# Kernel optimization log

Measured on AMD Instinct MI355X. Metric: run time of the kernel, lower is better.

Reference implementation:

```python
import jax, jax.numpy as jnp
import numpy as np

N_NODES = 100000
N_EDGES = 1600000
D_FEAT = 48
N_LAYERS = 3  # GCN(n_layers=3) builds exactly 3 GraphConv layers


def setup_inputs() -> dict:
    key = jax.random.key(0)
    k1, k2, k3 = jax.random.split(key, 3)
    features = jax.random.normal(k1, (N_NODES, D_FEAT), dtype=jnp.float32)
    src = jax.random.randint(k2, (N_EDGES,), 0, N_NODES, dtype=jnp.int32)
    dst = jax.random.randint(k3, (N_EDGES,), 0, N_NODES, dtype=jnp.int32)
    return {"features": features, "src": src, "dst": dst}


def reference(features, src, dst):
    # GraphConv(norm='none', weight=False, bias=False): h_v = sum_{u->v} h_u, then activation.
    # Layers 0..N_LAYERS-2 apply relu; the final layer has no activation.
    h = features
    for i in range(N_LAYERS):
        msgs = h[src]  # gather source features per edge: [E, D]
        h = jax.ops.segment_sum(msgs, dst, num_segments=N_NODES)  # scatter-add to dst
        if i < N_LAYERS - 1:
            h = jax.nn.relu(h)
    return h
```

## Files before the change

### kernel.cpp

```cpp
#include <hip/hip_runtime.h>

#define D 48
#define BSH 8
#define BN 256
#define NBMAX 400
#define CH 256
#define CAPT 5120
#define LOUTSZ 6400
#define PB 6400

typedef float v2f __attribute__((ext_vector_type(2)));

#if defined(__has_builtin)
#if __has_builtin(__builtin_amdgcn_cvt_pk_f32_fp8)
#define HAVE_HW_FP8 1
#endif
#if __has_builtin(__builtin_amdgcn_cvt_pk_fp8_f32)
#define HAVE_HW_FP8ENC 1
#endif
#endif

static __device__ inline unsigned int f2bf_rne(float x) {
    unsigned int u = __float_as_uint(x);
    return (u + 0x7FFFu + ((u >> 16) & 1u)) >> 16;
}
static __device__ inline unsigned int pack2(float lo, float hi) {
    return f2bf_rne(lo) | (f2bf_rne(hi) << 16);
}
static __device__ inline float bf_lo(unsigned int u) { return __uint_as_float(u << 16); }
static __device__ inline float bf_hi(unsigned int u) { return __uint_as_float(u & 0xFFFF0000u); }

static __device__ inline unsigned int f2fp8(float x) {
    unsigned int u = __float_as_uint(x);
    unsigned int s = (u >> 24) & 0x80u;
    unsigned int e = (u >> 23) & 0xFFu;
    unsigned int m = u & 0x7FFFFFu;
    if (e < 121u) return s;
    unsigned int m2 = m + 0x7FFFFu + ((m >> 20) & 1u);
    unsigned int carry = m2 >> 23;
    unsigned int e2 = e - 120u + carry;
    unsigned int b = s | (e2 << 3) | ((m2 >> 20) & 7u);
    if (e2 > 15u || (b & 0x7Fu) == 0x7Fu) b = s | 0x7Eu;
    return b;
}
static __device__ inline float fp8_dec(unsigned int b) {
    unsigned int bits = ((b & 0x80u) << 24) | (((b & 0x7Fu) << 20) + (120u << 23));
    float v = __uint_as_float(bits);
    return ((b & 0x7Fu) != 0u) ? v : 0.0f;
}
static __device__ inline unsigned int packfp8x4(float a, float b, float c, float d) {
#if HAVE_HW_FP8ENC
    int w = __builtin_amdgcn_cvt_pk_fp8_f32(a, b, 0, false);
    w = __builtin_amdgcn_cvt_pk_fp8_f32(c, d, w, true);
    return (unsigned int)w;
#else
    return f2fp8(a) | (f2fp8(b) << 8) | (f2fp8(c) << 16) | (f2fp8(d) << 24);
#endif
}


__global__ void k_front(const int* __restrict__ dst, const float* __restrict__ feat,
                        uint2* __restrict__ featq, uint2* __restrict__ h1q,
                        uint4* __restrict__ featb, int* __restrict__ btot,
                        int* __restrict__ cbase, int E, int NB, int CHE, int N) {
    int t = threadIdx.x;
    if (blockIdx.x < CH) {
        int c = blockIdx.x;
        __shared__ int h[NBMAX];
        for (int b = t; b < NB; b += 1024) h[b] = 0;
        __syncthreads();
        int lo = c * CHE, hi = min(lo + CHE, E);
        for (int i = lo + t; i < hi; i += 1024)
            atomicAdd(&h[dst[i] >> BSH], 1);
        __syncthreads();
        for (int b = t; b < NB; b += 1024)
            cbase[c * NB + b] = atomicAdd(&btot[b], h[b]);
    } else {
        if (blockIdx.x == CH && t < 8) {
            h1q[(size_t)N * 8 + t] = make_uint2(0u, 0u);
            featb[(size_t)N * 8 + t] = make_uint4(0u, 0u, 0u, 0u);
        }
        const float4* f4 = (const float4*)feat;
        int total = (N + 1) * 8;
        int i = (blockIdx.x - CH) * 1024 + t;
        int stride = 256 * 1024;
        for (; i < total; i += stride) {
            int node = i >> 3, c = i & 7;
            uint2 v = make_uint2(0u, 0u);
            if (c < 6 && node < N) {
                float4 a = f4[node * 12 + 2 * c];
                float4 b = f4[node * 12 + 2 * c + 1];
                v.x = f2fp8(a.x) | (f2fp8(a.y) << 8) | (f2fp8(a.z) << 16) | (f2fp8(a.w) << 24);
                v.y = f2fp8(b.x) | (f2fp8(b.y) << 8) | (f2fp8(b.z) << 16) | (f2fp8(b.w) << 24);
            }
            featq[i] = v;
        }
    }
}


__global__ void k_scatter(const int* __restrict__ src, const int* __restrict__ dst,
                          const int* __restrict__ btot, const int* __restrict__ cbase,
                          int* __restrict__ stage, int* __restrict__ bbase,
                          int E, int NB, int CHE) {
    int c = blockIdx.x;
    int t = threadIdx.x;
    __shared__ int wtot[8];
    __shared__ int cur[NBMAX];
    int w = t >> 6, ln = t & 63;
    int x = 0, v = 0;
    if (t < 448) {
        v = (t < NB) ? btot[t] : 0;
        x = v;
#pragma unroll
        for (int off = 1; off < 64; off <<= 1) {
            int u = __shfl_up(x, off);
            if (ln >= off) x += u;
        }
        if (ln == 63) wtot[w] = x;
    }
    __syncthreads();
    if (t == 0) {
        int a = 0;
        for (int k = 0; k < 7; k++) { int tmp = wtot[k]; wtot[k] = a; a += tmp; }
        wtot[7] = a;
    }
    __syncthreads();
    if (t < NB) {
        int excl = x - v + wtot[w];
        cur[t] = excl + cbase[c * NB + t];
        if (c == 0) bbase[t] = excl;
    }
    if (c == 0 && t == 0) bbase[NB] = wtot[7];
    __syncthreads();
    int lo = c * CHE, hi = min(lo + CHE, E);
    for (int i = lo + t; i < hi; i += 1024) {
        int s = src[i], d = dst[i];
        int p = atomicAdd(&cur[d >> BSH], 1);
        stage[p] = ((d & (BN - 1)) << 17) | s;
    }
}


__global__ void k_build(const int* __restrict__ stage, const int* __restrict__ bbase,
                        int* __restrict__ row_ptr, int* __restrict__ trips,
                        int* __restrict__ esrc, int N, int NB) {
    int b = blockIdx.x;
    int t = threadIdx.x;
    __shared__ int lbuf[CAPT];
    __shared__ int lout[LOUTSZ];
    __shared__ int hist[BN];
    __shared__ int cur[BN];
    __shared__ int wt[4];
    __shared__ int stot;
    int base = bbase[b];
    int cnt = min(bbase[b + 1] - base, CAPT);
    hist[t] = 0;
    __syncthreads();
    for (int i = t; i < cnt; i += 256) {
        int v = stage[base + i];
        lbuf[i] = v;
        atomicAdd(&hist[v >> 17], 1);
    }
    __syncthreads();
    int orig = hist[t];
    int pc = (orig + 7) & ~7;
    int w = t >> 6, ln = t & 63;
    int x = pc;
#pragma unroll
    for (int off = 1; off < 64; off <<= 1) {
        int u = __shfl_up(x, off);
        if (ln >= off) x += u;
    }
    if (ln == 63) wt[w] = x;
    __syncthreads();
    if (t == 0) {
        int a = 0;
        for (int k = 0; k < 4; k++) { int tmp = wt[k]; wt[k] = a; a += tmp; }
    }
    __syncthreads();
    int ppre = x - pc + wt[w];
    cur[t] = ppre;
    int node = (b << BSH) + t;
    if (node < N) { row_ptr[node] = b * PB + ppre; trips[node] = pc >> 3; }
    for (int k = orig; k < pc; k++) lout[ppre + k] = N;
    if (t == 255) stot = ppre + pc;
    __syncthreads();
    for (int i = t; i < cnt; i += 256) {
        int v = lbuf[i];
        int p = atomicAdd(&cur[v >> 17], 1);
        lout[p] = v & 0x1FFFF;
    }
    __syncthreads();
    int ptot = stot;
    for (int i = t; i < ptot; i += 256) esrc[b * PB + i] = lout[i];
}


#if HAVE_HW_FP8
#define DEC8(q) do { \
        v2f p0 = __builtin_amdgcn_cvt_pk_f32_fp8((int)(q).x, false); \
        v2f p1 = __builtin_amdgcn_cvt_pk_f32_fp8((int)(q).x, true); \
        v2f p2 = __builtin_amdgcn_cvt_pk_f32_fp8((int)(q).y, false); \
        v2f p3 = __builtin_amdgcn_cvt_pk_f32_fp8((int)(q).y, true); \
        a0 += p0.x; a1 += p0.y; a2 += p1.x; a3 += p1.y; \
        a4 += p2.x; a5 += p2.y; a6 += p3.x; a7 += p3.y; } while (0)
#else
#define DEC8(q) do { \
        a0 += fp8_dec((q).x & 0xFFu); a1 += fp8_dec(((q).x >> 8) & 0xFFu); \
        a2 += fp8_dec(((q).x >> 16) & 0xFFu); a3 += fp8_dec((q).x >> 24); \
        a4 += fp8_dec((q).y & 0xFFu); a5 += fp8_dec(((q).y >> 8) & 0xFFu); \
        a6 += fp8_dec(((q).y >> 16) & 0xFFu); a7 += fp8_dec((q).y >> 24); } while (0)
#endif

template <int OUTBF16>
__global__ void k_pullq(const uint2* __restrict__ hin, void* __restrict__ hout,
                        const int* __restrict__ row_ptr, const int* __restrict__ trips,
                        const int* __restrict__ esrc, int n) {
    int grp = threadIdx.x >> 4;
    int lane = threadIdx.x & 15;
    int side = lane >> 3;
    int sub = lane & 7;
    int node = blockIdx.x * 16 + grp;
    if (node >= n) return;
    int j = row_ptr[node];
    int nt = trips[node];
    float a0 = 0.f, a1 = 0.f, a2 = 0.f, a3 = 0.f, a4 = 0.f, a5 = 0.f, a6 = 0.f, a7 = 0.f;
    if (nt > 0) {
        int s0 = esrc[j + 0 + side], s1 = esrc[j + 2 + side];
        int s2 = esrc[j + 4 + side], s3 = esrc[j + 6 + side];
        for (; nt > 0; --nt) {
            uint2 q0 = hin[(size_t)s0 * 8 + sub];
            uint2 q1 = hin[(size_t)s1 * 8 + sub];
            uint2 q2 = hin[(size_t)s2 * 8 + sub];
            uint2 q3 = hin[(size_t)s3 * 8 + sub];
            j += 8;
            int n0 = esrc[j + 0 + side], n1 = esrc[j + 2 + side];
            int n2 = esrc[j + 4 + side], n3 = esrc[j + 6 + side];
            DEC8(q0); DEC8(q1); DEC8(q2); DEC8(q3);
            s0 = n0; s1 = n1; s2 = n2; s3 = n3;
        }
    }
    a0 += __shfl_xor(a0, 8); a1 += __shfl_xor(a1, 8);
    a2 += __shfl_xor(a2, 8); a3 += __shfl_xor(a3, 8);
    a4 += __shfl_xor(a4, 8); a5 += __shfl_xor(a5, 8);
    a6 += __shfl_xor(a6, 8); a7 += __shfl_xor(a7, 8);
    a0 = fmaxf(a0, 0.f); a1 = fmaxf(a1, 0.f); a2 = fmaxf(a2, 0.f); a3 = fmaxf(a3, 0.f);
    a4 = fmaxf(a4, 0.f); a5 = fmaxf(a5, 0.f); a6 = fmaxf(a6, 0.f); a7 = fmaxf(a7, 0.f);
    if (side != 0) return;
    if (OUTBF16) {
        uint4* o = (uint4*)hout + (size_t)node * 8 + sub;
        *o = make_uint4(pack2(a0, a1), pack2(a2, a3), pack2(a4, a5), pack2(a6, a7));
    } else {
        uint2* o = (uint2*)hout + (size_t)node * 8 + sub;
        *o = make_uint2(packfp8x4(a0, a1, a2, a3), packfp8x4(a4, a5, a6, a7));
    }
}
#undef DEC8


__global__ void k_pull(const uint4* __restrict__ hin, float* __restrict__ hout,
                       const int* __restrict__ row_ptr, const int* __restrict__ trips,
                       const int* __restrict__ esrc, int n) {
    int grp = threadIdx.x >> 4;
    int lane = threadIdx.x & 15;
    int side = lane >> 3;
    int sub = lane & 7;
    int node = blockIdx.x * 16 + grp;
    if (node >= n) return;
    int j = row_ptr[node];
    int nt = trips[node];
    float a0 = 0.f, a1 = 0.f, a2 = 0.f, a3 = 0.f, a4 = 0.f, a5 = 0.f, a6 = 0.f, a7 = 0.f;
    if (nt > 0) {
        int s0 = esrc[j + 0 + side], s1 = esrc[j + 2 + side];
        int s2 = esrc[j + 4 + side], s3 = esrc[j + 6 + side];
        for (; nt > 0; --nt) {
            uint4 q0 = hin[(size_t)s0 * 8 + sub];
            uint4 q1 = hin[(size_t)s1 * 8 + sub];
            uint4 q2 = hin[(size_t)s2 * 8 + sub];
            uint4 q3 = hin[(size_t)s3 * 8 + sub];
            j += 8;
            int n0 = esrc[j + 0 + side], n1 = esrc[j + 2 + side];
            int n2 = esrc[j + 4 + side], n3 = esrc[j + 6 + side];
            a0 += bf_lo(q0.x); a1 += bf_hi(q0.x); a2 += bf_lo(q0.y); a3 += bf_hi(q0.y);
            a4 += bf_lo(q0.z); a5 += bf_hi(q0.z); a6 += bf_lo(q0.w); a7 += bf_hi(q0.w);
            a0 += bf_lo(q1.x); a1 += bf_hi(q1.x); a2 += bf_lo(q1.y); a3 += bf_hi(q1.y);
            a4 += bf_lo(q1.z); a5 += bf_hi(q1.z); a6 += bf_lo(q1.w); a7 += bf_hi(q1.w);
            a0 += bf_lo(q2.x); a1 += bf_hi(q2.x); a2 += bf_lo(q2.y); a3 += bf_hi(q2.y);
            a4 += bf_lo(q2.z); a5 += bf_hi(q2.z); a6 += bf_lo(q2.w); a7 += bf_hi(q2.w);
            a0 += bf_lo(q3.x); a1 += bf_hi(q3.x); a2 += bf_lo(q3.y); a3 += bf_hi(q3.y);
            a4 += bf_lo(q3.z); a5 += bf_hi(q3.z); a6 += bf_lo(q3.w); a7 += bf_hi(q3.w);
            s0 = n0; s1 = n1; s2 = n2; s3 = n3;
        }
    }
    a0 += __shfl_xor(a0, 8); a1 += __shfl_xor(a1, 8);
    a2 += __shfl_xor(a2, 8); a3 += __shfl_xor(a3, 8);
    a4 += __shfl_xor(a4, 8); a5 += __shfl_xor(a5, 8);
    a6 += __shfl_xor(a6, 8); a7 += __shfl_xor(a7, 8);
    if (side != 0) return;
    if (sub < 6) {
        float* o = hout + (size_t)node * D + 8 * sub;
        *(float4*)(o)     = make_float4(a0, a1, a2, a3);
        *(float4*)(o + 4) = make_float4(a4, a5, a6, a7);
    }
}

extern "C" void kernel_launch(void* const* d_in, const int* in_sizes, int n_in,
                              void* d_out, int out_size, void* d_ws, size_t ws_size,
                              hipStream_t stream) {
    const float* feat = (const float*)d_in[0];
    const int* src = (const int*)d_in[1];
    const int* dst = (const int*)d_in[2];
    int N = in_sizes[0] / D;
    int E = in_sizes[1];
    int NB = (N + BN - 1) >> BSH;
    int CHE = (E + CH - 1) / CH;

    char* ws = (char*)d_ws;
    int*   btot    = (int*)(ws + ((size_t)0 << 10));
    int*   bbase   = (int*)(ws + ((size_t)64 << 10));
    int*   cbase   = (int*)(ws + ((size_t)128 << 10));
    int*   row_ptr = (int*)(ws + ((size_t)640 << 10));
    int*   trips   = (int*)(ws + ((size_t)1152 << 10));
    int*   esrc    = (int*)(ws + ((size_t)2 << 20));
    uint2* featq   = (uint2*)(ws + ((size_t)13 << 20));
    uint4* featb   = (uint4*)(ws + ((size_t)20 << 20));
    int*   stage   = (int*)(ws + ((size_t)33 << 20));
    uint2* h1q     = (uint2*)(ws + ((size_t)33 << 20));

    hipMemsetAsync(btot, 0, (size_t)NB * sizeof(int), stream);

    k_front<<<CH + 256, 1024, 0, stream>>>(dst, feat, featq, h1q, featb, btot, cbase, E, NB, CHE, N);
    k_scatter<<<CH, 1024, 0, stream>>>(src, dst, btot, cbase, stage, bbase, E, NB, CHE);
    k_build<<<NB, 256, 0, stream>>>(stage, bbase, row_ptr, trips, esrc, N, NB);

    int pg = (N + 15) / 16;
    k_pullq<0><<<pg, 256, 0, stream>>>(featq, h1q, row_ptr, trips, esrc, N);
    k_pullq<1><<<pg, 256, 0, stream>>>(h1q, featb, row_ptr, trips, esrc, N);
    k_pull<<<pg, 256, 0, stream>>>(featb, (float*)d_out, row_ptr, trips, esrc, N);
}
```

Before: 179.5 us.

## Fuse bucket count and scatter into one kernel with fixed-capacity bucket slots

Replaces the two-pass count-then-prefix-then-scatter with a single kernel that reserves per-bucket offsets atomically and scatters straight into fixed CAPT-sized bucket regions. This drops one kernel launch, the cbase/bbase arrays and the global prefix scan. Edges beyond CAPT per bucket are silently dropped, which was already the truncation limit in the build step. The pull kernels also load edge source indices as int4 vectors rather than four scalar loads, which changes which edges each half-group reads.

```diff
diff --git a/kernel.cpp b/kernel.cpp
--- a/kernel.cpp
+++ b/kernel.cpp
@@ -59,14 +59,16 @@
 }
 
 
-__global__ void k_front(const int* __restrict__ dst, const float* __restrict__ feat,
+__global__ void k_fscat(const int* __restrict__ src, const int* __restrict__ dst,
+                        const float* __restrict__ feat,
                         uint2* __restrict__ featq, uint2* __restrict__ h1q,
                         uint4* __restrict__ featb, int* __restrict__ btot,
-                        int* __restrict__ cbase, int E, int NB, int CHE, int N) {
+                        int* __restrict__ stage, int E, int NB, int CHE, int N) {
     int t = threadIdx.x;
     if (blockIdx.x < CH) {
         int c = blockIdx.x;
         __shared__ int h[NBMAX];
+        __shared__ int curl[NBMAX];
         for (int b = t; b < NB; b += 1024) h[b] = 0;
         __syncthreads();
         int lo = c * CHE, hi = min(lo + CHE, E);
@@ -74,7 +76,15 @@
             atomicAdd(&h[dst[i] >> BSH], 1);
         __syncthreads();
         for (int b = t; b < NB; b += 1024)
-            cbase[c * NB + b] = atomicAdd(&btot[b], h[b]);
+            curl[b] = b * CAPT + atomicAdd(&btot[b], h[b]);
+        __syncthreads();
+        for (int i = lo + t; i < hi; i += 1024) {
+            int s = src[i], d = dst[i];
+            int bkt = d >> BSH;
+            int p = atomicAdd(&curl[bkt], 1);
+            if (p < (bkt + 1) * CAPT)
+                stage[p] = ((d & (BN - 1)) << 17) | s;
+        }
     } else {
         if (blockIdx.x == CH && t < 8) {
             h1q[(size_t)N * 8 + t] = make_uint2(0u, 0u);
@@ -85,11 +95,11 @@
         int i = (blockIdx.x - CH) * 1024 + t;
         int stride = 256 * 1024;
         for (; i < total; i += stride) {
-            int node = i >> 3, c = i & 7;
+            int node = i >> 3, cc = i & 7;
             uint2 v = make_uint2(0u, 0u);
-            if (c < 6 && node < N) {
-                float4 a = f4[node * 12 + 2 * c];
-                float4 b = f4[node * 12 + 2 * c + 1];
+            if (cc < 6 && node < N) {
+                float4 a = f4[node * 12 + 2 * cc];
+                float4 b = f4[node * 12 + 2 * cc + 1];
                 v.x = f2fp8(a.x) | (f2fp8(a.y) << 8) | (f2fp8(a.z) << 16) | (f2fp8(a.w) << 24);
                 v.y = f2fp8(b.x) | (f2fp8(b.y) << 8) | (f2fp8(b.z) << 16) | (f2fp8(b.w) << 24);
             }
@@ -99,50 +109,7 @@
 }
 
 
-__global__ void k_scatter(const int* __restrict__ src, const int* __restrict__ dst,
-                          const int* __restrict__ btot, const int* __restrict__ cbase,
-                          int* __restrict__ stage, int* __restrict__ bbase,
-                          int E, int NB, int CHE) {
-    int c = blockIdx.x;
-    int t = threadIdx.x;
-    __shared__ int wtot[8];
-    __shared__ int cur[NBMAX];
-    int w = t >> 6, ln = t & 63;
-    int x = 0, v = 0;
-    if (t < 448) {
-        v = (t < NB) ? btot[t] : 0;
-        x = v;
-#pragma unroll
-        for (int off = 1; off < 64; off <<= 1) {
-            int u = __shfl_up(x, off);
-            if (ln >= off) x += u;
-        }
-        if (ln == 63) wtot[w] = x;
-    }
-    __syncthreads();
-    if (t == 0) {
-        int a = 0;
-        for (int k = 0; k < 7; k++) { int tmp = wtot[k]; wtot[k] = a; a += tmp; }
-        wtot[7] = a;
-    }
-    __syncthreads();
-    if (t < NB) {
-        int excl = x - v + wtot[w];
-        cur[t] = excl + cbase[c * NB + t];
-        if (c == 0) bbase[t] = excl;
-    }
-    if (c == 0 && t == 0) bbase[NB] = wtot[7];
-    __syncthreads();
-    int lo = c * CHE, hi = min(lo + CHE, E);
-    for (int i = lo + t; i < hi; i += 1024) {
-        int s = src[i], d = dst[i];
-        int p = atomicAdd(&cur[d >> BSH], 1);
-        stage[p] = ((d & (BN - 1)) << 17) | s;
-    }
-}
-
-
-__global__ void k_build(const int* __restrict__ stage, const int* __restrict__ bbase,
+__global__ void k_build(const int* __restrict__ stage, const int* __restrict__ btot,
                         int* __restrict__ row_ptr, int* __restrict__ trips,
                         int* __restrict__ esrc, int N, int NB) {
     int b = blockIdx.x;
@@ -153,8 +120,8 @@
     __shared__ int cur[BN];
     __shared__ int wt[4];
     __shared__ int stot;
-    int base = bbase[b];
-    int cnt = min(bbase[b + 1] - base, CAPT);
+    int base = b * CAPT;
+    int cnt = min(btot[b], CAPT);
     hist[t] = 0;
     __syncthreads();
     for (int i = t; i < cnt; i += 256) {
@@ -227,18 +194,16 @@
     int nt = trips[node];
     float a0 = 0.f, a1 = 0.f, a2 = 0.f, a3 = 0.f, a4 = 0.f, a5 = 0.f, a6 = 0.f, a7 = 0.f;
     if (nt > 0) {
-        int s0 = esrc[j + 0 + side], s1 = esrc[j + 2 + side];
-        int s2 = esrc[j + 4 + side], s3 = esrc[j + 6 + side];
+        int4 s4 = *(const int4*)(esrc + j + 4 * side);
         for (; nt > 0; --nt) {
-            uint2 q0 = hin[(size_t)s0 * 8 + sub];
-            uint2 q1 = hin[(size_t)s1 * 8 + sub];
-            uint2 q2 = hin[(size_t)s2 * 8 + sub];
-            uint2 q3 = hin[(size_t)s3 * 8 + sub];
+            uint2 q0 = hin[(size_t)s4.x * 8 + sub];
+            uint2 q1 = hin[(size_t)s4.y * 8 + sub];
+            uint2 q2 = hin[(size_t)s4.z * 8 + sub];
+            uint2 q3 = hin[(size_t)s4.w * 8 + sub];
             j += 8;
-            int n0 = esrc[j + 0 + side], n1 = esrc[j + 2 + side];
-            int n2 = esrc[j + 4 + side], n3 = esrc[j + 6 + side];
+            int4 n4 = *(const int4*)(esrc + j + 4 * side);
             DEC8(q0); DEC8(q1); DEC8(q2); DEC8(q3);
-            s0 = n0; s1 = n1; s2 = n2; s3 = n3;
+            s4 = n4;
         }
     }
     a0 += __shfl_xor(a0, 8); a1 += __shfl_xor(a1, 8);
@@ -272,16 +237,14 @@
     int nt = trips[node];
     float a0 = 0.f, a1 = 0.f, a2 = 0.f, a3 = 0.f, a4 = 0.f, a5 = 0.f, a6 = 0.f, a7 = 0.f;
     if (nt > 0) {
-        int s0 = esrc[j + 0 + side], s1 = esrc[j + 2 + side];
-        int s2 = esrc[j + 4 + side], s3 = esrc[j + 6 + side];
+        int4 s4 = *(const int4*)(esrc + j + 4 * side);
         for (; nt > 0; --nt) {
-            uint4 q0 = hin[(size_t)s0 * 8 + sub];
-            uint4 q1 = hin[(size_t)s1 * 8 + sub];
-            uint4 q2 = hin[(size_t)s2 * 8 + sub];
-            uint4 q3 = hin[(size_t)s3 * 8 + sub];
+            uint4 q0 = hin[(size_t)s4.x * 8 + sub];
+            uint4 q1 = hin[(size_t)s4.y * 8 + sub];
+            uint4 q2 = hin[(size_t)s4.z * 8 + sub];
+            uint4 q3 = hin[(size_t)s4.w * 8 + sub];
             j += 8;
-            int n0 = esrc[j + 0 + side], n1 = esrc[j + 2 + side];
-            int n2 = esrc[j + 4 + side], n3 = esrc[j + 6 + side];
+            int4 n4 = *(const int4*)(esrc + j + 4 * side);
             a0 += bf_lo(q0.x); a1 += bf_hi(q0.x); a2 += bf_lo(q0.y); a3 += bf_hi(q0.y);
             a4 += bf_lo(q0.z); a5 += bf_hi(q0.z); a6 += bf_lo(q0.w); a7 += bf_hi(q0.w);
             a0 += bf_lo(q1.x); a1 += bf_hi(q1.x); a2 += bf_lo(q1.y); a3 += bf_hi(q1.y);
@@ -290,7 +253,7 @@
             a4 += bf_lo(q2.z); a5 += bf_hi(q2.z); a6 += bf_lo(q2.w); a7 += bf_hi(q2.w);
             a0 += bf_lo(q3.x); a1 += bf_hi(q3.x); a2 += bf_lo(q3.y); a3 += bf_hi(q3.y);
             a4 += bf_lo(q3.z); a5 += bf_hi(q3.z); a6 += bf_lo(q3.w); a7 += bf_hi(q3.w);
-            s0 = n0; s1 = n1; s2 = n2; s3 = n3;
+            s4 = n4;
         }
     }
     a0 += __shfl_xor(a0, 8); a1 += __shfl_xor(a1, 8);
@@ -318,21 +281,18 @@
 
     char* ws = (char*)d_ws;
     int*   btot    = (int*)(ws + ((size_t)0 << 10));
-    int*   bbase   = (int*)(ws + ((size_t)64 << 10));
-    int*   cbase   = (int*)(ws + ((size_t)128 << 10));
     int*   row_ptr = (int*)(ws + ((size_t)640 << 10));
     int*   trips   = (int*)(ws + ((size_t)1152 << 10));
     int*   esrc    = (int*)(ws + ((size_t)2 << 20));
     uint2* featq   = (uint2*)(ws + ((size_t)13 << 20));
     uint4* featb   = (uint4*)(ws + ((size_t)20 << 20));
     int*   stage   = (int*)(ws + ((size_t)33 << 20));
-    uint2* h1q     = (uint2*)(ws + ((size_t)33 << 20));
+    uint2* h1q     = (uint2*)(ws + ((size_t)42 << 20));
 
     hipMemsetAsync(btot, 0, (size_t)NB * sizeof(int), stream);
 
-    k_front<<<CH + 256, 1024, 0, stream>>>(dst, feat, featq, h1q, featb, btot, cbase, E, NB, CHE, N);
-    k_scatter<<<CH, 1024, 0, stream>>>(src, dst, btot, cbase, stage, bbase, E, NB, CHE);
-    k_build<<<NB, 256, 0, stream>>>(stage, bbase, row_ptr, trips, esrc, N, NB);
+    k_fscat<<<CH + 256, 1024, 0, stream>>>(src, dst, feat, featq, h1q, featb, btot, stage, E, NB, CHE, N);
+    k_build<<<NB, 256, 0, stream>>>(stage, btot, row_ptr, trips, esrc, N, NB);
 
     int pg = (N + 15) / 16;
     k_pullq<0><<<pg, 256, 0, stream>>>(featq, h1q, row_ptr, trips, esrc, N);
```

Result: no change. 181.6 us (+1.2%).
